# Kernel optimization log

Hardware: AMD Instinct MI355X
Metric: run time of the kernel (lower is better)

The kernel has to match this reference:

```python
import jax, jax.numpy as jnp
import numpy as np

INPUT_HASH_SIZE = 4_000_000
ZCH_SIZE = 400_000
EMB_DIM = 128
N_IDS = 1_000_000


def _remap(ids, mch_sorted):
    """MCH-style ID remapping: binary-search raw id in the sorted ZCH id table.
    Matched ids map to their slot index; unmatched ids map to the last
    (collision/overflow) slot zch_size - 1."""
    zch_size = mch_sorted.shape[0]
    pos = jnp.searchsorted(mch_sorted, ids)
    pos = jnp.clip(pos, 0, zch_size - 1)
    hit = mch_sorted[pos] == ids
    return jnp.where(hit, pos, zch_size - 1)


def setup_inputs() -> dict:
    key = jax.random.key(0)
    k0, k1, k2, k3, k4, k5 = jax.random.split(key, 6)
    ids_0 = jax.random.randint(k0, (N_IDS,), 0, INPUT_HASH_SIZE, dtype=jnp.int64)
    ids_1 = jax.random.randint(k1, (N_IDS,), 0, INPUT_HASH_SIZE, dtype=jnp.int64)
    mch_ids_0 = jnp.sort(jax.random.randint(k2, (ZCH_SIZE,), 0, INPUT_HASH_SIZE, dtype=jnp.int64))
    mch_ids_1 = jnp.sort(jax.random.randint(k3, (ZCH_SIZE,), 0, INPUT_HASH_SIZE, dtype=jnp.int64))
    emb_0 = jax.random.normal(k4, (ZCH_SIZE, EMB_DIM), dtype=jnp.float32)
    emb_1 = jax.random.normal(k5, (ZCH_SIZE, EMB_DIM), dtype=jnp.float32)
    return {"ids_0": ids_0, "ids_1": ids_1, "mch_ids_0": mch_ids_0,
            "mch_ids_1": mch_ids_1, "emb_0": emb_0, "emb_1": emb_1}


def reference(ids_0, ids_1, mch_ids_0, mch_ids_1, emb_0, emb_1):
    # managed-collision remap per feature
    remapped_0 = _remap(ids_0, mch_ids_0)  # [N]
    remapped_1 = _remap(ids_1, mch_ids_1)  # [N]
    # embedding gather per feature -> [N, D]
    v0 = jnp.take(emb_0, remapped_0, axis=0)
    v1 = jnp.take(emb_1, remapped_1, axis=0)
    # pred = cat along dim 0, loss = mean
    pred = jnp.concatenate([v0, v1], axis=0)  # [2N, D]
    loss = pred.mean()
    return loss, remapped_0, remapped_1
```

## Files before the change

### kernel.cpp

```cpp
#include <hip/hip_runtime.h>
#include <stdint.h>

#define N_IDS     1000000
#define ZCH       400000
#define EMB_DIM   128
#define TOTAL     (2 * N_IDS)
#define HASH_SZ   4000000
#define BLOCK     256
#define GRID      ((TOTAL + BLOCK - 1) / BLOCK)
#define OVF       (ZCH - 1)


__global__ __launch_bounds__(256) void init_lut_kernel(int4* __restrict__ lut)
{
    int t = blockIdx.x * blockDim.x + threadIdx.x;
    if (t < (2 * HASH_SZ) / 4)
        lut[t] = make_int4(OVF, OVF, OVF, OVF);
}

__global__ __launch_bounds__(256) void scatter_lut_kernel(
    const int* __restrict__ mch0, const int* __restrict__ mch1,
    int* __restrict__ lut0, int* __restrict__ lut1)
{
    int t = blockIdx.x * blockDim.x + threadIdx.x;
    if (t >= 2 * ZCH) return;
    const int feat = t >= ZCH;
    const int s    = feat ? (t - ZCH) : t;
    const int* __restrict__ mch = feat ? mch1 : mch0;
    int* __restrict__ lut       = feat ? lut1 : lut0;
    const int v = mch[s];
    if (s == 0 || mch[s - 1] != v)
        lut[v] = s;
}

__global__ __launch_bounds__(BLOCK) void remap_loss_kernel(
    const int* __restrict__ ids0, const int* __restrict__ ids1,
    const float* __restrict__ emb0, const float* __restrict__ emb1,
    const int* __restrict__ lut0, const int* __restrict__ lut1,
    float* __restrict__ out,
    float* __restrict__ partials)
{
    const int gid  = blockIdx.x * BLOCK + threadIdx.x;
    const int lane = threadIdx.x & 63;
    const int wave = threadIdx.x >> 6;

    float accl = 0.0f;

    const bool active = (gid < TOTAL);
    if (active) {
        const int feat = gid >= N_IDS;
        const int i    = feat ? (gid - N_IDS) : gid;
        const int id   = (feat ? ids1 : ids0)[i];
        const float* __restrict__ emb = feat ? emb1 : emb0;

        const int rem = (feat ? lut1 : lut0)[id];

        out[1 + gid] = (float)rem;

        const unsigned long long ovf = __ballot(rem == OVF);
        const int novf = __popcll(ovf);
        if (novf) {
            const float2* __restrict__ row =
                (const float2*)(emb + (size_t)OVF * EMB_DIM);
            float2 v = row[lane];
            float s = v.x + v.y;
            #pragma unroll
            for (int o = 32; o > 0; o >>= 1)
                s += __shfl_xor(s, o, 64);
            if (lane == 0) accl += (float)novf * s;
        }

        const int half = lane >> 5;
        const int l32  = lane & 31;
        unsigned long long hits = ~ovf;
        #pragma unroll 1
        while (hits) {
            int j0 = __ffsll(hits) - 1;
            hits &= hits - 1;
            const bool dup = (hits == 0);
            int j1 = dup ? j0 : (__ffsll(hits) - 1);
            if (!dup) hits &= hits - 1;
            int r = __shfl(rem, half ? j1 : j0, 64);
            const float4* __restrict__ row =
                (const float4*)(emb + (size_t)r * EMB_DIM);
            float4 v = row[l32];
            float s4 = (v.x + v.y) + (v.z + v.w);
            accl += (half && dup) ? 0.0f : s4;
        }
    }

    #pragma unroll
    for (int o = 32; o > 0; o >>= 1)
        accl += __shfl_down(accl, o, 64);

    __shared__ float wsum[BLOCK / 64];
    if (lane == 0) wsum[wave] = accl;
    __syncthreads();
    if (threadIdx.x == 0) {
        float s = 0.0f;
        #pragma unroll
        for (int w = 0; w < BLOCK / 64; ++w) s += wsum[w];
        partials[blockIdx.x] = s;
    }
}

__global__ __launch_bounds__(256) void finalize_kernel(
    const float* __restrict__ partials, float* __restrict__ out)
{
    __shared__ double sh[256];
    double s = 0.0;
    for (int i = threadIdx.x; i < GRID; i += 256)
        s += (double)partials[i];
    sh[threadIdx.x] = s;
    __syncthreads();
    #pragma unroll
    for (int stride = 128; stride > 0; stride >>= 1) {
        if (threadIdx.x < stride) sh[threadIdx.x] += sh[threadIdx.x + stride];
        __syncthreads();
    }
    if (threadIdx.x == 0)
        out[0] = (float)(sh[0] / ((double)TOTAL * (double)EMB_DIM));
}

extern "C" void kernel_launch(void* const* d_in, const int* in_sizes, int n_in,
                              void* d_out, int out_size, void* d_ws, size_t ws_size,
                              hipStream_t stream) {
    const int*   ids0 = (const int*)d_in[0];
    const int*   ids1 = (const int*)d_in[1];
    const int*   mch0 = (const int*)d_in[2];
    const int*   mch1 = (const int*)d_in[3];
    const float* emb0 = (const float*)d_in[4];
    const float* emb1 = (const float*)d_in[5];

    float* out      = (float*)d_out;
    int*   lut0     = (int*)d_ws;
    int*   lut1     = lut0 + HASH_SZ;
    float* partials = (float*)(lut1 + HASH_SZ);

    init_lut_kernel<<<((2 * HASH_SZ / 4) + 255) / 256, 256, 0, stream>>>(
        (int4*)d_ws);
    scatter_lut_kernel<<<(2 * ZCH + 255) / 256, 256, 0, stream>>>(
        mch0, mch1, lut0, lut1);
    remap_loss_kernel<<<GRID, BLOCK, 0, stream>>>(
        ids0, ids1, emb0, emb1, lut0, lut1, out, partials);
    finalize_kernel<<<1, 256, 0, stream>>>(partials, out);
}
```

Before: 383.2 us.

## Compress remap LUT to byte offsets plus per-256-bucket base table

Replaces the 4-byte-per-entry direct lookup table with a 1-byte offset table plus an int base array indexed by id>>8. Each base entry is found by binary search in the sorted ZCH ids, and 0xFF marks a miss. This cuts the LUT memory footprint and the init fill by 4x, so it should fit better in cache and need less bandwidth for the random lookups. In exchange it adds binary searches during the build and an extra base load per id, and it assumes fewer than 255 distinct ids fall in any 256-wide bucket.

```diff
diff --git a/kernel.cpp b/kernel.cpp
--- a/kernel.cpp
+++ b/kernel.cpp
@@ -9,34 +9,57 @@
 #define BLOCK     256
 #define GRID      ((TOTAL + BLOCK - 1) / BLOCK)
 #define OVF       (ZCH - 1)
+#define NBASE     16384
 
 
-__global__ __launch_bounds__(256) void init_lut_kernel(int4* __restrict__ lut)
+__global__ __launch_bounds__(256) void init_lut_kernel(uint4* __restrict__ lut)
 {
     int t = blockIdx.x * blockDim.x + threadIdx.x;
-    if (t < (2 * HASH_SZ) / 4)
-        lut[t] = make_int4(OVF, OVF, OVF, OVF);
+    if (t < (2 * HASH_SZ) / 16)
+        lut[t] = make_uint4(0xFFFFFFFFu, 0xFFFFFFFFu, 0xFFFFFFFFu, 0xFFFFFFFFu);
 }
 
-__global__ __launch_bounds__(256) void scatter_lut_kernel(
+__device__ __forceinline__ int lower_bound_dev(const int* __restrict__ a, int target)
+{
+    int lo = 0, hi = ZCH;
+    while (lo < hi) {
+        int mid = (lo + hi) >> 1;
+        if (a[mid] < target) lo = mid + 1; else hi = mid;
+    }
+    return lo;
+}
+
+__global__ __launch_bounds__(256) void build_lut_kernel(
     const int* __restrict__ mch0, const int* __restrict__ mch1,
-    int* __restrict__ lut0, int* __restrict__ lut1)
+    unsigned char* __restrict__ lut0, unsigned char* __restrict__ lut1,
+    int* __restrict__ base0, int* __restrict__ base1)
 {
     int t = blockIdx.x * blockDim.x + threadIdx.x;
-    if (t >= 2 * ZCH) return;
-    const int feat = t >= ZCH;
-    const int s    = feat ? (t - ZCH) : t;
-    const int* __restrict__ mch = feat ? mch1 : mch0;
-    int* __restrict__ lut       = feat ? lut1 : lut0;
-    const int v = mch[s];
-    if (s == 0 || mch[s - 1] != v)
-        lut[v] = s;
+    if (t < 2 * ZCH) {
+        const int feat = t >= ZCH;
+        const int s    = feat ? (t - ZCH) : t;
+        const int* __restrict__ mch = feat ? mch1 : mch0;
+        const int v = mch[s];
+        if (s == 0 || mch[s - 1] != v) {
+            const int lo = lower_bound_dev(mch, v & ~255);
+            (feat ? lut1 : lut0)[v] = (unsigned char)(s - lo);
+        }
+    } else {
+        int u = t - 2 * ZCH;
+        if (u < 2 * NBASE) {
+            const int feat = u >= NBASE;
+            const int b    = feat ? (u - NBASE) : u;
+            const int* __restrict__ mch = feat ? mch1 : mch0;
+            (feat ? base1 : base0)[b] = lower_bound_dev(mch, b << 8);
+        }
+    }
 }
 
 __global__ __launch_bounds__(BLOCK) void remap_loss_kernel(
     const int* __restrict__ ids0, const int* __restrict__ ids1,
     const float* __restrict__ emb0, const float* __restrict__ emb1,
-    const int* __restrict__ lut0, const int* __restrict__ lut1,
+    const unsigned char* __restrict__ lut0, const unsigned char* __restrict__ lut1,
+    const int* __restrict__ base0, const int* __restrict__ base1,
     float* __restrict__ out,
     float* __restrict__ partials)
 {
@@ -53,7 +76,9 @@
         const int id   = (feat ? ids1 : ids0)[i];
         const float* __restrict__ emb = feat ? emb1 : emb0;
 
-        const int rem = (feat ? lut1 : lut0)[id];
+        const unsigned int w = (feat ? lut1 : lut0)[id];
+        const int          b = (feat ? base1 : base0)[id >> 8];
+        const int rem = (w == 0xFFu) ? OVF : (b + (int)w);
 
         out[1 + gid] = (float)rem;
 
@@ -132,16 +157,18 @@
     const float* emb0 = (const float*)d_in[4];
     const float* emb1 = (const float*)d_in[5];
 
-    float* out      = (float*)d_out;
-    int*   lut0     = (int*)d_ws;
-    int*   lut1     = lut0 + HASH_SZ;
-    float* partials = (float*)(lut1 + HASH_SZ);
+    float* out = (float*)d_out;
+    unsigned char* lut0 = (unsigned char*)d_ws;
+    unsigned char* lut1 = lut0 + HASH_SZ;
+    int*   base0    = (int*)(lut1 + HASH_SZ);
+    int*   base1    = base0 + NBASE;
+    float* partials = (float*)(base1 + NBASE);
 
-    init_lut_kernel<<<((2 * HASH_SZ / 4) + 255) / 256, 256, 0, stream>>>(
-        (int4*)d_ws);
-    scatter_lut_kernel<<<(2 * ZCH + 255) / 256, 256, 0, stream>>>(
-        mch0, mch1, lut0, lut1);
+    init_lut_kernel<<<((2 * HASH_SZ / 16) + 255) / 256, 256, 0, stream>>>(
+        (uint4*)d_ws);
+    build_lut_kernel<<<(2 * ZCH + 2 * NBASE + 255) / 256, 256, 0, stream>>>(
+        mch0, mch1, lut0, lut1, base0, base1);
     remap_loss_kernel<<<GRID, BLOCK, 0, stream>>>(
-        ids0, ids1, emb0, emb1, lut0, lut1, out, partials);
+        ids0, ids1, emb0, emb1, lut0, lut1, base0, base1, out, partials);
     finalize_kernel<<<1, 256, 0, stream>>>(partials, out);
 }
```

After: 389.0 us. About the same (+1.5%).

## Replace dense lookup-table remap with per-thread binary search over sorted ids

Applied to the files above, without the earlier changes.

Drops the two kernels that filled a 32 MB lookup table and scattered slot indices into it. Each thread now binary-searches its id in the sorted ZCH table directly. This removes the large memset and scatter traffic plus two launches, at the cost of about 19 dependent, divergent global loads per id. The upper levels of the search tree should stay in cache.

```diff
diff --git a/kernel.cpp b/kernel.cpp
--- a/kernel.cpp
+++ b/kernel.cpp
@@ -11,32 +11,10 @@
 #define OVF       (ZCH - 1)
 
 
-__global__ __launch_bounds__(256) void init_lut_kernel(int4* __restrict__ lut)
-{
-    int t = blockIdx.x * blockDim.x + threadIdx.x;
-    if (t < (2 * HASH_SZ) / 4)
-        lut[t] = make_int4(OVF, OVF, OVF, OVF);
-}
-
-__global__ __launch_bounds__(256) void scatter_lut_kernel(
-    const int* __restrict__ mch0, const int* __restrict__ mch1,
-    int* __restrict__ lut0, int* __restrict__ lut1)
-{
-    int t = blockIdx.x * blockDim.x + threadIdx.x;
-    if (t >= 2 * ZCH) return;
-    const int feat = t >= ZCH;
-    const int s    = feat ? (t - ZCH) : t;
-    const int* __restrict__ mch = feat ? mch1 : mch0;
-    int* __restrict__ lut       = feat ? lut1 : lut0;
-    const int v = mch[s];
-    if (s == 0 || mch[s - 1] != v)
-        lut[v] = s;
-}
-
 __global__ __launch_bounds__(BLOCK) void remap_loss_kernel(
     const int* __restrict__ ids0, const int* __restrict__ ids1,
+    const int* __restrict__ mch0, const int* __restrict__ mch1,
     const float* __restrict__ emb0, const float* __restrict__ emb1,
-    const int* __restrict__ lut0, const int* __restrict__ lut1,
     float* __restrict__ out,
     float* __restrict__ partials)
 {
@@ -51,9 +29,15 @@
         const int feat = gid >= N_IDS;
         const int i    = feat ? (gid - N_IDS) : gid;
         const int id   = (feat ? ids1 : ids0)[i];
+        const int* __restrict__ mch = feat ? mch1 : mch0;
         const float* __restrict__ emb = feat ? emb1 : emb0;
 
-        const int rem = (feat ? lut1 : lut0)[id];
+        int lo = 0, hi = ZCH;
+        while (lo < hi) {
+            const int mid = (lo + hi) >> 1;
+            if (mch[mid] < id) lo = mid + 1; else hi = mid;
+        }
+        const int rem = (lo < ZCH && mch[lo] == id) ? lo : OVF;
 
         out[1 + gid] = (float)rem;
 
@@ -133,15 +117,9 @@
     const float* emb1 = (const float*)d_in[5];
 
     float* out      = (float*)d_out;
-    int*   lut0     = (int*)d_ws;
-    int*   lut1     = lut0 + HASH_SZ;
-    float* partials = (float*)(lut1 + HASH_SZ);
+    float* partials = (float*)d_ws;
 
-    init_lut_kernel<<<((2 * HASH_SZ / 4) + 255) / 256, 256, 0, stream>>>(
-        (int4*)d_ws);
-    scatter_lut_kernel<<<(2 * ZCH + 255) / 256, 256, 0, stream>>>(
-        mch0, mch1, lut0, lut1);
     remap_loss_kernel<<<GRID, BLOCK, 0, stream>>>(
-        ids0, ids1, emb0, emb1, lut0, lut1, out, partials);
+        ids0, ids1, mch0, mch1, emb0, emb1, out, partials);
     finalize_kernel<<<1, 256, 0, stream>>>(partials, out);
 }
```

New measurement: 460.5 us. 20.2% more time.
